# Kernel optimization log

Hardware: AMD Instinct MI355X
Metric: run time of the kernel (lower is better)

## Reference

```python
import jax, jax.numpy as jnp
import numpy as np

DIM = 256; HEADS = 8; DK = 64; DV = 64; FH = 32; FW = 32; B = 16
INK = HEADS * DK; INV = HEADS * DV; N = FH * FW
SCALE = DK ** -0.5; EPS = 1e-5


def _pos_indices():
    pos = np.stack(np.meshgrid(np.arange(FH), np.arange(FW), indexing='ij'), axis=-1).reshape(-1, 2)
    rel = np.abs(pos[:, None, :] - pos[None, :, :])  # [N,N,2]
    return jnp.asarray(rel[..., 0] * FW + rel[..., 1], jnp.int32)  # [N,N]


def _bn(x, g, b, m, v):
    # eval-mode BatchNorm2d over channel axis 1
    s = (g / jnp.sqrt(v + EPS))
    return x * s[None, :, None, None] + (b - m * s)[None, :, None, None]


def setup_inputs() -> dict:
    key = jax.random.key(0)
    ks = jax.random.split(key, 24)
    f32 = jnp.float32
    def bn_params(k, c):
        k1, k2, k3, k4 = jax.random.split(k, 4)
        return (jax.random.normal(k1, (c,), f32) * 0.1 + 1.0,
                jax.random.normal(k2, (c,), f32) * 0.1,
                jax.random.normal(k3, (c,), f32) * 0.1,
                jax.random.uniform(k4, (c,), f32) + 0.5)
    gq, bq, mq, vq = bn_params(ks[1], INK)
    gk, bk, mk, vk = bn_params(ks[3], INK)
    gv, bv, mv, vv = bn_params(ks[5], INV)
    go, bo, mo, vo = bn_params(ks[7], DIM)
    return {
        'x': jax.random.normal(ks[0], (B, DIM, FH, FW), f32),
        'wq': jax.random.normal(ks[2], (INK, DIM), f32) * (DIM ** -0.5),
        'gq': gq, 'bq': bq, 'mq': mq, 'vq': vq,
        'wk': jax.random.normal(ks[4], (INK, DIM), f32) * (DIM ** -0.5),
        'gk': gk, 'bk': bk, 'mk': mk, 'vk': vk,
        'wv': jax.random.normal(ks[6], (INV, DIM), f32) * (DIM ** -0.5),
        'gv': gv, 'bv': bv, 'mv': mv, 'vv': vv,
        'emb': jax.random.normal(ks[8], (N, HEADS), f32) * 0.02,
        'w_out': jax.random.normal(ks[9], (DIM, INV), f32) * (INV ** -0.5),
        'b_out': jax.random.normal(ks[10], (DIM,), f32) * 0.02,
        'go': go, 'bo': bo, 'mo': mo, 'vo': vo,
        'pos_indices': _pos_indices(),
    }


def reference(x, wq, gq, bq, mq, vq, wk, gk, bk, mk, vk, wv, gv, bv, mv, vv,
              emb, w_out, b_out, go, bo, mo, vo, pos_indices):
    b = x.shape[0]
    # 1x1 conv == channel matmul
    q = _bn(jnp.einsum('bchw,oc->bohw', x, wq), gq, bq, mq, vq)
    k = _bn(jnp.einsum('bchw,oc->bohw', x, wk), gk, bk, mk, vk)
    v = _bn(jnp.einsum('bchw,oc->bohw', x, wv), gv, bv, mv, vv)
    # 'b (h d) x y -> b h (x y) d'
    def split_heads(t, d):
        return t.reshape(b, HEADS, d, N).transpose(0, 1, 3, 2)
    q = split_heads(q, DK); k = split_heads(k, DK); v = split_heads(v, DV)
    dots = jnp.einsum('bhid,bhjd->bhij', q, k) * SCALE  # [b,h,N,N]
    bias = emb[pos_indices]                               # [N,N,h] gather
    dots = dots + jnp.transpose(bias, (2, 0, 1))[None] / SCALE
    attn = jax.nn.softmax(dots, axis=-1)
    out = jnp.einsum('bhij,bhjd->bhid', attn, v)
    out = out.transpose(0, 1, 3, 2).reshape(b, INV, FH, FW)  # 'b h (x y) d -> b (h d) x y'
    hs = out * jnp.clip(out + 3.0, 0.0, 6.0) / 6.0           # Hardswish
    y = jnp.einsum('bchw,oc->bohw', hs, w_out) + b_out[None, :, None, None]
    return _bn(y, go, bo, mo, vo)
```

## Files before the change

kernel.cpp:

```cpp
#include <hip/hip_runtime.h>

typedef __attribute__((ext_vector_type(4))) float f32x4;
typedef __attribute__((ext_vector_type(8))) _Float16 f16x8;
typedef __attribute__((ext_vector_type(4))) _Float16 f16x4;

static __device__ __forceinline__ f32x4 mfma16f(f16x8 a, f16x8 b, f32x4 c) {
    return __builtin_amdgcn_mfma_f32_16x16x32_f16(a, b, c, 0, 0, 0);
}

__global__ void split_w4(const float* __restrict__ s0, const float* __restrict__ s1,
                         const float* __restrict__ s2, const float* __restrict__ s3,
                         _Float16* __restrict__ d0h, _Float16* __restrict__ d0l,
                         _Float16* __restrict__ d1h, _Float16* __restrict__ d1l,
                         _Float16* __restrict__ d2h, _Float16* __restrict__ d2l,
                         _Float16* __restrict__ d3h, _Float16* __restrict__ d3l) {
    const int seg = blockIdx.x >> 9;
    const int i = (blockIdx.x & 511) * 256 + threadIdx.x;
    const float* src = (seg == 0) ? s0 : (seg == 1) ? s1 : (seg == 2) ? s2 : s3;
    _Float16* dh = (seg == 0) ? d0h : (seg == 1) ? d1h : (seg == 2) ? d2h : d3h;
    _Float16* dl = (seg == 0) ? d0l : (seg == 1) ? d1l : (seg == 2) ? d2l : d3l;
    const float f = src[i];
    const _Float16 h = (_Float16)f;
    dh[i] = h;
    dl[i] = (_Float16)(f - (float)h);
}

__global__ __launch_bounds__(256) void xsplit_t(
    const float* __restrict__ x, _Float16* __restrict__ xth, _Float16* __restrict__ xtl)
{
    __shared__ float lt[32][36];
    const int t = threadIdx.x;
    const int c0 = blockIdx.x * 32, hw0 = blockIdx.y * 32, b = blockIdx.z;
    {
        const int cl = t >> 3, hw4 = (t & 7) * 4;
        *(f32x4*)&lt[cl][hw4] = *(const f32x4*)&x[((size_t)(b * 256 + c0 + cl)) * 1024 + hw0 + hw4];
    }
    __syncthreads();
    {
        const int hwl = t >> 3, c4 = (t & 7) * 4;
        f16x4 hv, lv;
#pragma unroll
        for (int e = 0; e < 4; ++e) {
            const float f = lt[c4 + e][hwl];
            const _Float16 h = (_Float16)f;
            hv[e] = h;
            lv[e] = (_Float16)(f - (float)h);
        }
        const size_t off = ((size_t)(b * 1024 + hw0 + hwl)) * 256 + c0 + c4;
        *(f16x4*)(xth + off) = hv;
        *(f16x4*)(xtl + off) = lv;
    }
}

__global__ __launch_bounds__(256) void qkv_mfma(
    const _Float16* __restrict__ xth, const _Float16* __restrict__ xtl,
    const _Float16* __restrict__ wqh, const _Float16* __restrict__ wql,
    const _Float16* __restrict__ wkh, const _Float16* __restrict__ wkl,
    const _Float16* __restrict__ wvh, const _Float16* __restrict__ wvl,
    const float* __restrict__ gq, const float* __restrict__ bq, const float* __restrict__ mq, const float* __restrict__ vq,
    const float* __restrict__ gk, const float* __restrict__ bk, const float* __restrict__ mk, const float* __restrict__ vk,
    const float* __restrict__ gv, const float* __restrict__ bv, const float* __restrict__ mv, const float* __restrict__ vv,
    _Float16* __restrict__ qh, _Float16* __restrict__ ql,
    _Float16* __restrict__ kh, _Float16* __restrict__ kl,
    _Float16* __restrict__ vt)
{
    __shared__ _Float16 Ah[128][72];
    __shared__ _Float16 Al[128][72];
    __shared__ float sc_l[128], tc_l[128];

    const int t = threadIdx.x;
    const int bn = blockIdx.x;
    const int m0 = blockIdx.y * 128;
    const int proj = bn >> 2;
    const int o0 = (bn & 3) * 128;
    const int bimg = m0 >> 10;
    const int nb = m0 & 1023;

    const _Float16* Wh = (proj == 0) ? wqh : (proj == 1) ? wkh : wvh;
    const _Float16* Wl = (proj == 0) ? wql : (proj == 1) ? wkl : wvl;
    const float* G  = (proj == 0) ? gq : (proj == 1) ? gk : gv;
    const float* Bt = (proj == 0) ? bq : (proj == 1) ? bk : bv;
    const float* Mn = (proj == 0) ? mq : (proj == 1) ? mk : mv;
    const float* Vr = (proj == 0) ? vq : (proj == 1) ? vk : vv;

    if (t < 128) {
        const int o = o0 + t;
        float s = G[o] / sqrtf(Vr[o] + 1e-5f);
        float tt = Bt[o] - Mn[o] * s;
        if (proj == 0) { s *= 0.125f; tt *= 0.125f; }
        sc_l[t] = s; tc_l[t] = tt;
    }

    const int wave = t >> 6, lane = t & 63;
    const int quad = lane >> 4, l16 = lane & 15;
    const int wm = (wave >> 1) * 64, wn = (wave & 1) * 64;

    f32x4 acc[4][4] = {};

    for (int c0 = 0; c0 < 256; c0 += 64) {
        __syncthreads();
        {
            int r = t >> 3;
            const int cs = (t & 7) * 8;
#pragma unroll
            for (int p = 0; p < 4; ++p, r += 32) {
                const size_t off = ((size_t)(bimg * 1024 + nb + r)) * 256 + c0 + cs;
                *(f16x8*)&Ah[r][cs] = *(const f16x8*)(xth + off);
                *(f16x8*)&Al[r][cs] = *(const f16x8*)(xtl + off);
            }
        }
        __syncthreads();
#pragma unroll
        for (int kk = 0; kk < 2; ++kk) {
            f16x8 ah[4], al[4], bh[4], bl[4];
#pragma unroll
            for (int mi = 0; mi < 4; ++mi) {
                ah[mi] = *(const f16x8*)&Ah[wm + mi * 16 + l16][kk * 32 + quad * 8];
                al[mi] = *(const f16x8*)&Al[wm + mi * 16 + l16][kk * 32 + quad * 8];
            }
#pragma unroll
            for (int nj = 0; nj < 4; ++nj) {
                const size_t off = ((size_t)(o0 + wn + nj * 16 + l16)) * 256 + c0 + kk * 32 + quad * 8;
                bh[nj] = *(const f16x8*)(Wh + off);
                if (proj < 2) bl[nj] = *(const f16x8*)(Wl + off);
            }
            if (proj < 2) {
#pragma unroll
                for (int nj = 0; nj < 4; ++nj)
#pragma unroll
                    for (int mi = 0; mi < 4; ++mi) {
                        acc[nj][mi] = mfma16f(bh[nj], ah[mi], acc[nj][mi]);
                        acc[nj][mi] = mfma16f(bh[nj], al[mi], acc[nj][mi]);
                        acc[nj][mi] = mfma16f(bl[nj], ah[mi], acc[nj][mi]);
                    }
            } else {
#pragma unroll
                for (int mi = 0; mi < 4; ++mi)
#pragma unroll
                    for (int nj = 0; nj < 4; ++nj) {
                        acc[mi][nj] = mfma16f(ah[mi], bh[nj], acc[mi][nj]);
                        acc[mi][nj] = mfma16f(al[mi], bh[nj], acc[mi][nj]);
                    }
            }
        }
    }

    if (proj < 2) {
        _Float16* Oh = (proj == 0) ? qh : kh;
        _Float16* Ol = (proj == 0) ? ql : kl;
#pragma unroll
        for (int nj = 0; nj < 4; ++nj) {
            const int olb = wn + nj * 16 + quad * 4;
            const int ob = o0 + olb;
            const int head = ob >> 6, d0 = ob & 63;
#pragma unroll
            for (int mi = 0; mi < 4; ++mi) {
                const int n = nb + wm + mi * 16 + l16;
                f16x4 hv, lv;
#pragma unroll
                for (int rr = 0; rr < 4; ++rr) {
                    const float val = acc[nj][mi][rr] * sc_l[olb + rr] + tc_l[olb + rr];
                    const _Float16 h = (_Float16)val;
                    hv[rr] = h;
                    lv[rr] = (_Float16)(val - (float)h);
                }
                const size_t off = (((size_t)(bimg * 8 + head)) * 1024 + n) * 64 + d0;
                *(f16x4*)(Oh + off) = hv;
                *(f16x4*)(Ol + off) = lv;
            }
        }
    } else {
#pragma unroll
        for (int nj = 0; nj < 4; ++nj) {
            const int olb = wn + nj * 16 + l16;
            const int o = o0 + olb;
            const int head = o >> 6, d = o & 63;
            const float s = sc_l[olb], tt = tc_l[olb];
#pragma unroll
            for (int mi = 0; mi < 4; ++mi) {
                const int n0 = nb + wm + mi * 16 + quad * 4;
                f16x4 v4;
#pragma unroll
                for (int rr = 0; rr < 4; ++rr) v4[rr] = (_Float16)(acc[mi][nj][rr] * s + tt);
                *(f16x4*)(vt + (((size_t)(bimg * 8 + head)) * 64 + d) * 1024 + n0) = v4;
            }
        }
    }
}

__global__ __launch_bounds__(256, 3) void attn_mfma(
    const _Float16* __restrict__ qh, const _Float16* __restrict__ ql,
    const _Float16* __restrict__ kh, const _Float16* __restrict__ kl,
    const _Float16* __restrict__ vt,
    const float* __restrict__ emb,
    _Float16* __restrict__ hsh)
{
    __shared__ float    emb_s[1024];
    __shared__ _Float16 kth[64][72], ktl[64][72];
    __shared__ _Float16 vts[64][72];
    __shared__ _Float16 pt[128][76];

    const int t = threadIdx.x;
    const int bid = blockIdx.x;
    const int bh = bid & 127, qb = bid >> 7;
    const int b = bh >> 3, h = bh & 7;
    const int wave = t >> 6, lane = t & 63;
    const int quad = lane >> 4, l16 = lane & 15;
    const int q0 = qb * 128 + wave * 32;
    const float L2E = 1.44269504f;

    for (int i = t; i < 1024; i += 256) emb_s[i] = (8.0f * emb[i * 8 + h] - 12.0f) * L2E;

    const size_t base = (size_t)bh * 65536;

    f16x8 qfh[2][2], qfl[2][2];
#pragma unroll
    for (int mi = 0; mi < 2; ++mi)
#pragma unroll
        for (int kk = 0; kk < 2; ++kk) {
            const size_t off = base + (size_t)(q0 + mi * 16 + l16) * 64 + kk * 32 + quad * 8;
            qfh[mi][kk] = *(const f16x8*)(qh + off);
            qfl[mi][kk] = *(const f16x8*)(ql + off);
        }

    int xiv[2][4], dy0[2][4], dy1[2][4];
#pragma unroll
    for (int mi = 0; mi < 2; ++mi)
#pragma unroll
        for (int r = 0; r < 4; ++r) {
            const int ig = q0 + mi * 16 + quad * 4 + r;
            const int xi = ig >> 5, yi = ig & 31;
            xiv[mi][r] = xi;
            dy0[mi][r] = abs(yi - l16);
            dy1[mi][r] = abs(yi - 16 - l16);
        }

    const int sr = t >> 3;
    const int scs = (t & 7) * 8;
    const int rv = t >> 2;
    const int cv = (t & 3) * 16;

    f16x8 pkh[2], pkl[2], pvv[2];
#pragma unroll
    for (int p = 0; p < 2; ++p) {
        const size_t koff = base + (size_t)(p * 32 + sr) * 64 + scs;
        pkh[p] = *(const f16x8*)(kh + koff);
        pkl[p] = *(const f16x8*)(kl + koff);
        pvv[p] = *(const f16x8*)(vt + base + (size_t)rv * 1024 + cv + p * 8);
    }

    f32x4 ao[2][4] = {};
    float lsum[2][4] = {};

    for (int jb = 0; jb < 16; ++jb) {
        __syncthreads();
#pragma unroll
        for (int p = 0; p < 2; ++p) {
            *(f16x8*)&kth[p * 32 + sr][scs] = pkh[p];
            *(f16x8*)&ktl[p * 32 + sr][scs] = pkl[p];
            *(f16x8*)&vts[rv][cv + p * 8] = pvv[p];
        }
        __syncthreads();
        if (jb < 15) {
#pragma unroll
            for (int p = 0; p < 2; ++p) {
                const size_t koff = base + (size_t)((jb + 1) * 64 + p * 32 + sr) * 64 + scs;
                pkh[p] = *(const f16x8*)(kh + koff);
                pkl[p] = *(const f16x8*)(kl + koff);
                pvv[p] = *(const f16x8*)(vt + base + (size_t)rv * 1024 + (jb + 1) * 64 + cv + p * 8);
            }
        }

        f32x4 as[2][4] = {};
#pragma unroll
        for (int kk = 0; kk < 2; ++kk) {
            f16x8 kfh[4], kfl[4];
#pragma unroll
            for (int nj = 0; nj < 4; ++nj) {
                kfh[nj] = *(const f16x8*)&kth[nj * 16 + l16][kk * 32 + quad * 8];
                kfl[nj] = *(const f16x8*)&ktl[nj * 16 + l16][kk * 32 + quad * 8];
            }
#pragma unroll
            for (int mi = 0; mi < 2; ++mi)
#pragma unroll
                for (int nj = 0; nj < 4; ++nj) {
                    as[mi][nj] = mfma16f(qfh[mi][kk], kfh[nj], as[mi][nj]);
                    as[mi][nj] = mfma16f(qfh[mi][kk], kfl[nj], as[mi][nj]);
                    as[mi][nj] = mfma16f(qfl[mi][kk], kfh[nj], as[mi][nj]);
                }
        }

        const int xj0 = jb * 2, xj1 = jb * 2 + 1;
#pragma unroll
        for (int mi = 0; mi < 2; ++mi) {
#pragma unroll
            for (int r = 0; r < 4; ++r) {
                const int dxa = abs(xiv[mi][r] - xj0) << 5;
                const int dxb = abs(xiv[mi][r] - xj1) << 5;
                const int prow = wave * 32 + mi * 16 + quad * 4 + r;
                const float p0 = exp2f(fmaf(as[mi][0][r], L2E, emb_s[dxa + dy0[mi][r]]));
                const float p1 = exp2f(fmaf(as[mi][1][r], L2E, emb_s[dxa + dy1[mi][r]]));
                const float p2 = exp2f(fmaf(as[mi][2][r], L2E, emb_s[dxb + dy0[mi][r]]));
                const float p3 = exp2f(fmaf(as[mi][3][r], L2E, emb_s[dxb + dy1[mi][r]]));
                lsum[mi][r] += (p0 + p1) + (p2 + p3);
                pt[prow][0 * 16 + l16] = (_Float16)p0;
                pt[prow][1 * 16 + l16] = (_Float16)p1;
                pt[prow][2 * 16 + l16] = (_Float16)p2;
                pt[prow][3 * 16 + l16] = (_Float16)p3;
            }
        }

#pragma unroll
        for (int kk = 0; kk < 2; ++kk) {
            f16x8 pa[2], vf[4];
#pragma unroll
            for (int mi = 0; mi < 2; ++mi)
                pa[mi] = *(const f16x8*)&pt[wave * 32 + mi * 16 + l16][kk * 32 + quad * 8];
#pragma unroll
            for (int dj = 0; dj < 4; ++dj)
                vf[dj] = *(const f16x8*)&vts[dj * 16 + l16][kk * 32 + quad * 8];
#pragma unroll
            for (int mi = 0; mi < 2; ++mi)
#pragma unroll
                for (int dj = 0; dj < 4; ++dj)
                    ao[mi][dj] = mfma16f(pa[mi], vf[dj], ao[mi][dj]);
        }
    }

#pragma unroll
    for (int mi = 0; mi < 2; ++mi) {
#pragma unroll
        for (int r = 0; r < 4; ++r) {
            float l = lsum[mi][r];
#pragma unroll
            for (int msk = 1; msk < 16; msk <<= 1)
                l += __shfl_xor(l, msk, 64);
            const float inv = 1.0f / l;
            const int ig = q0 + mi * 16 + quad * 4 + r;
#pragma unroll
            for (int dj = 0; dj < 4; ++dj) {
                const float o = ao[mi][dj][r] * inv;
                const float hsw = o * fminf(fmaxf(o + 3.0f, 0.0f), 6.0f) * (1.0f / 6.0f);
                hsh[((size_t)(b * 1024 + ig)) * 512 + h * 64 + dj * 16 + l16] = (_Float16)hsw;
            }
        }
    }
}

__global__ __launch_bounds__(256) void out_mfma(
    const _Float16* __restrict__ hsh,
    const _Float16* __restrict__ woh, const _Float16* __restrict__ wol,
    const float* __restrict__ b_out, const float* __restrict__ go, const float* __restrict__ bo,
    const float* __restrict__ mo, const float* __restrict__ vo, float* __restrict__ y)
{
    __shared__ _Float16 Ah[64][136];

    const int t = threadIdx.x;
    const int m0 = blockIdx.x * 64;
    const int o0 = blockIdx.y * 128;
    const int bimg = m0 >> 10, nb = m0 & 1023;
    const int wave = t >> 6, lane = t & 63;
    const int quad = lane >> 4, l16 = lane & 15;
    const int wm = (wave >> 1) * 32, wn = (wave & 1) * 64;

    f32x4 acc[2][4] = {};

    for (int c0 = 0; c0 < 512; c0 += 128) {
        __syncthreads();
        {
            const int cs = (t & 7) * 16;
#pragma unroll
            for (int p = 0; p < 2; ++p) {
                const int r = (t >> 3) + p * 32;
                *(f16x8*)&Ah[r][cs]     = *(const f16x8*)(hsh + ((size_t)(m0 + r)) * 512 + c0 + cs);
                *(f16x8*)&Ah[r][cs + 8] = *(const f16x8*)(hsh + ((size_t)(m0 + r)) * 512 + c0 + cs + 8);
            }
        }
        __syncthreads();
#pragma unroll
        for (int kk = 0; kk < 4; ++kk) {
            f16x8 ah[2], bh[4], bl[4];
#pragma unroll
            for (int mi = 0; mi < 2; ++mi)
                ah[mi] = *(const f16x8*)&Ah[wm + mi * 16 + l16][kk * 32 + quad * 8];
#pragma unroll
            for (int nj = 0; nj < 4; ++nj) {
                const size_t off = ((size_t)(o0 + wn + nj * 16 + l16)) * 512 + c0 + kk * 32 + quad * 8;
                bh[nj] = *(const f16x8*)(woh + off);
                bl[nj] = *(const f16x8*)(wol + off);
            }
#pragma unroll
            for (int mi = 0; mi < 2; ++mi)
#pragma unroll
                for (int nj = 0; nj < 4; ++nj) {
                    acc[mi][nj] = mfma16f(ah[mi], bh[nj], acc[mi][nj]);
                    acc[mi][nj] = mfma16f(ah[mi], bl[nj], acc[mi][nj]);
                }
        }
    }

#pragma unroll
    for (int nj = 0; nj < 4; ++nj) {
        const int o = o0 + wn + nj * 16 + l16;
        const float s = go[o] / sqrtf(vo[o] + 1e-5f);
        const float tt = bo[o] - mo[o] * s;
        const float bf = b_out[o];
#pragma unroll
        for (int mi = 0; mi < 2; ++mi) {
            const int hw = nb + wm + mi * 16 + quad * 4;
            f32x4 v4;
#pragma unroll
            for (int rr = 0; rr < 4; ++rr) v4[rr] = (acc[mi][nj][rr] + bf) * s + tt;
            *(f32x4*)&y[((size_t)(bimg * 256 + o)) * 1024 + hw] = v4;
        }
    }
}

extern "C" void kernel_launch(void* const* d_in, const int* in_sizes, int n_in,
                              void* d_out, int out_size, void* d_ws, size_t ws_size,
                              hipStream_t stream) {
    const float* x     = (const float*)d_in[0];
    const float* wq    = (const float*)d_in[1];
    const float* gq    = (const float*)d_in[2];
    const float* bq    = (const float*)d_in[3];
    const float* mq    = (const float*)d_in[4];
    const float* vq    = (const float*)d_in[5];
    const float* wk    = (const float*)d_in[6];
    const float* gk    = (const float*)d_in[7];
    const float* bk    = (const float*)d_in[8];
    const float* mk    = (const float*)d_in[9];
    const float* vk    = (const float*)d_in[10];
    const float* wv    = (const float*)d_in[11];
    const float* gv    = (const float*)d_in[12];
    const float* bv    = (const float*)d_in[13];
    const float* mv    = (const float*)d_in[14];
    const float* vv    = (const float*)d_in[15];
    const float* emb   = (const float*)d_in[16];
    const float* w_out = (const float*)d_in[17];
    const float* b_out = (const float*)d_in[18];
    const float* go    = (const float*)d_in[19];
    const float* bo    = (const float*)d_in[20];
    const float* mo    = (const float*)d_in[21];
    const float* vo    = (const float*)d_in[22];

    _Float16* us = (_Float16*)d_ws;
    _Float16* xth = us;
    _Float16* xtl = us + 4194304;
    _Float16* hsh = us;
    _Float16* wsp = us + 16777216;
    _Float16* wqh = wsp,            *wql = wsp + 131072;
    _Float16* wkh = wsp + 262144,   *wkl = wsp + 393216;
    _Float16* wvh = wsp + 524288,   *wvl = wsp + 655360;
    _Float16* woh = wsp + 786432,   *wol = wsp + 917504;
    _Float16* qv  = us + 17825792;
    _Float16* qhw = qv,             *qlw = qv + 8388608;
    _Float16* khw = qv + 16777216,  *klw = qv + 25165824;
    _Float16* vtw = qv + 33554432;

    split_w4<<<2048, 256, 0, stream>>>(wq, wk, wv, w_out,
                                       wqh, wql, wkh, wkl, wvh, wvl, woh, wol);

    xsplit_t<<<dim3(8, 32, 16), 256, 0, stream>>>(x, xth, xtl);

    qkv_mfma<<<dim3(12, 128), 256, 0, stream>>>(
        xth, xtl, wqh, wql, wkh, wkl, wvh, wvl,
        gq, bq, mq, vq, gk, bk, mk, vk, gv, bv, mv, vv,
        qhw, qlw, khw, klw, vtw);

    attn_mfma<<<1024, 256, 0, stream>>>(
        qhw, qlw, khw, klw, vtw, emb, hsh);

    out_mfma<<<dim3(256, 2), 256, 0, stream>>>(
        hsh, woh, wol, b_out, go, bo, mo, vo, (float*)d_out);
}
```

Baseline: 332.9 us.

## Drop K low-part split in attention, merge prep kernels, prefetch out weights

```diff
diff --git a/kernel.cpp b/kernel.cpp
--- a/kernel.cpp
+++ b/kernel.cpp
@@ -8,47 +8,51 @@
     return __builtin_amdgcn_mfma_f32_16x16x32_f16(a, b, c, 0, 0, 0);
 }
 
-__global__ void split_w4(const float* __restrict__ s0, const float* __restrict__ s1,
-                         const float* __restrict__ s2, const float* __restrict__ s3,
-                         _Float16* __restrict__ d0h, _Float16* __restrict__ d0l,
-                         _Float16* __restrict__ d1h, _Float16* __restrict__ d1l,
-                         _Float16* __restrict__ d2h, _Float16* __restrict__ d2l,
-                         _Float16* __restrict__ d3h, _Float16* __restrict__ d3l) {
-    const int seg = blockIdx.x >> 9;
-    const int i = (blockIdx.x & 511) * 256 + threadIdx.x;
-    const float* src = (seg == 0) ? s0 : (seg == 1) ? s1 : (seg == 2) ? s2 : s3;
-    _Float16* dh = (seg == 0) ? d0h : (seg == 1) ? d1h : (seg == 2) ? d2h : d3h;
-    _Float16* dl = (seg == 0) ? d0l : (seg == 1) ? d1l : (seg == 2) ? d2l : d3l;
-    const float f = src[i];
-    const _Float16 h = (_Float16)f;
-    dh[i] = h;
-    dl[i] = (_Float16)(f - (float)h);
-}
-
-__global__ __launch_bounds__(256) void xsplit_t(
-    const float* __restrict__ x, _Float16* __restrict__ xth, _Float16* __restrict__ xtl)
+__global__ __launch_bounds__(256) void prep(
+    const float* __restrict__ x,
+    const float* __restrict__ s0, const float* __restrict__ s1,
+    const float* __restrict__ s2, const float* __restrict__ s3,
+    _Float16* __restrict__ d0h, _Float16* __restrict__ d0l,
+    _Float16* __restrict__ d1h, _Float16* __restrict__ d1l,
+    _Float16* __restrict__ d2h, _Float16* __restrict__ d2l,
+    _Float16* __restrict__ d3h, _Float16* __restrict__ d3l,
+    _Float16* __restrict__ xth, _Float16* __restrict__ xtl)
 {
     __shared__ float lt[32][36];
     const int t = threadIdx.x;
-    const int c0 = blockIdx.x * 32, hw0 = blockIdx.y * 32, b = blockIdx.z;
-    {
-        const int cl = t >> 3, hw4 = (t & 7) * 4;
-        *(f32x4*)&lt[cl][hw4] = *(const f32x4*)&x[((size_t)(b * 256 + c0 + cl)) * 1024 + hw0 + hw4];
-    }
-    __syncthreads();
-    {
-        const int hwl = t >> 3, c4 = (t & 7) * 4;
-        f16x4 hv, lv;
-#pragma unroll
-        for (int e = 0; e < 4; ++e) {
-            const float f = lt[c4 + e][hwl];
-            const _Float16 h = (_Float16)f;
-            hv[e] = h;
-            lv[e] = (_Float16)(f - (float)h);
-        }
-        const size_t off = ((size_t)(b * 1024 + hw0 + hwl)) * 256 + c0 + c4;
-        *(f16x4*)(xth + off) = hv;
-        *(f16x4*)(xtl + off) = lv;
+    const int bid = blockIdx.x;
+    if (bid < 2048) {
+        const int seg = bid >> 9;
+        const int i = (bid & 511) * 256 + t;
+        const float* src = (seg == 0) ? s0 : (seg == 1) ? s1 : (seg == 2) ? s2 : s3;
+        _Float16* dh = (seg == 0) ? d0h : (seg == 1) ? d1h : (seg == 2) ? d2h : d3h;
+        _Float16* dl = (seg == 0) ? d0l : (seg == 1) ? d1l : (seg == 2) ? d2l : d3l;
+        const float f = src[i];
+        const _Float16 h = (_Float16)f;
+        dh[i] = h;
+        dl[i] = (_Float16)(f - (float)h);
+    } else {
+        const int bid2 = bid - 2048;
+        const int c0 = (bid2 & 7) * 32, hw0 = ((bid2 >> 3) & 31) * 32, b = bid2 >> 8;
+        {
+            const int cl = t >> 3, hw4 = (t & 7) * 4;
+            *(f32x4*)&lt[cl][hw4] = *(const f32x4*)&x[((size_t)(b * 256 + c0 + cl)) * 1024 + hw0 + hw4];
+        }
+        __syncthreads();
+        {
+            const int hwl = t >> 3, c4 = (t & 7) * 4;
+            f16x4 hv, lv;
+#pragma unroll
+            for (int e = 0; e < 4; ++e) {
+                const float f = lt[c4 + e][hwl];
+                const _Float16 h = (_Float16)f;
+                hv[e] = h;
+                lv[e] = (_Float16)(f - (float)h);
+            }
+            const size_t off = ((size_t)(b * 1024 + hw0 + hwl)) * 256 + c0 + c4;
+            *(f16x4*)(xth + off) = hv;
+            *(f16x4*)(xtl + off) = lv;
+        }
     }
 }
 
@@ -61,7 +65,7 @@
     const float* __restrict__ gk, const float* __restrict__ bk, const float* __restrict__ mk, const float* __restrict__ vk,
     const float* __restrict__ gv, const float* __restrict__ bv, const float* __restrict__ mv, const float* __restrict__ vv,
     _Float16* __restrict__ qh, _Float16* __restrict__ ql,
-    _Float16* __restrict__ kh, _Float16* __restrict__ kl,
+    _Float16* __restrict__ kh,
     _Float16* __restrict__ vt)
 {
     __shared__ _Float16 Ah[128][72];
@@ -147,7 +151,6 @@
 
     if (proj < 2) {
         _Float16* Oh = (proj == 0) ? qh : kh;
-        _Float16* Ol = (proj == 0) ? ql : kl;
 #pragma unroll
         for (int nj = 0; nj < 4; ++nj) {
             const int olb = wn + nj * 16 + quad * 4;
@@ -166,7 +169,7 @@
                 }
                 const size_t off = (((size_t)(bimg * 8 + head)) * 1024 + n) * 64 + d0;
                 *(f16x4*)(Oh + off) = hv;
-                *(f16x4*)(Ol + off) = lv;
+                if (proj == 0) *(f16x4*)(ql + off) = lv;
             }
         }
     } else {
@@ -190,14 +193,14 @@
 
 __global__ __launch_bounds__(256, 3) void attn_mfma(
     const _Float16* __restrict__ qh, const _Float16* __restrict__ ql,
-    const _Float16* __restrict__ kh, const _Float16* __restrict__ kl,
+    const _Float16* __restrict__ kh,
     const _Float16* __restrict__ vt,
     const float* __restrict__ emb,
     _Float16* __restrict__ hsh)
 {
     __shared__ float    emb_s[1024];
-    __shared__ _Float16 kth[64][72], ktl[64][72];
-    __shared__ _Float16 vts[64][72];
+    __shared__ _Float16 kth[64][76];
+    __shared__ _Float16 vts[64][76];
     __shared__ _Float16 pt[128][76];
 
     const int t = threadIdx.x;
@@ -240,12 +243,10 @@
     const int rv = t >> 2;
     const int cv = (t & 3) * 16;
 
-    f16x8 pkh[2], pkl[2], pvv[2];
+    f16x8 pkh[2], pvv[2];
 #pragma unroll
     for (int p = 0; p < 2; ++p) {
-        const size_t koff = base + (size_t)(p * 32 + sr) * 64 + scs;
-        pkh[p] = *(const f16x8*)(kh + koff);
-        pkl[p] = *(const f16x8*)(kl + koff);
+        pkh[p] = *(const f16x8*)(kh + base + (size_t)(p * 32 + sr) * 64 + scs);
         pvv[p] = *(const f16x8*)(vt + base + (size_t)rv * 1024 + cv + p * 8);
     }
 
@@ -257,16 +258,13 @@
 #pragma unroll
         for (int p = 0; p < 2; ++p) {
             *(f16x8*)&kth[p * 32 + sr][scs] = pkh[p];
-            *(f16x8*)&ktl[p * 32 + sr][scs] = pkl[p];
             *(f16x8*)&vts[rv][cv + p * 8] = pvv[p];
         }
         __syncthreads();
         if (jb < 15) {
 #pragma unroll
             for (int p = 0; p < 2; ++p) {
-                const size_t koff = base + (size_t)((jb + 1) * 64 + p * 32 + sr) * 64 + scs;
-                pkh[p] = *(const f16x8*)(kh + koff);
-                pkl[p] = *(const f16x8*)(kl + koff);
+                pkh[p] = *(const f16x8*)(kh + base + (size_t)((jb + 1) * 64 + p * 32 + sr) * 64 + scs);
                 pvv[p] = *(const f16x8*)(vt + base + (size_t)rv * 1024 + (jb + 1) * 64 + cv + p * 8);
             }
         }
@@ -274,18 +272,15 @@
         f32x4 as[2][4] = {};
 #pragma unroll
         for (int kk = 0; kk < 2; ++kk) {
-            f16x8 kfh[4], kfl[4];
-#pragma unroll
-            for (int nj = 0; nj < 4; ++nj) {
+            f16x8 kfh[4];
+#pragma unroll
+            for (int nj = 0; nj < 4; ++nj)
                 kfh[nj] = *(const f16x8*)&kth[nj * 16 + l16][kk * 32 + quad * 8];
-                kfl[nj] = *(const f16x8*)&ktl[nj * 16 + l16][kk * 32 + quad * 8];
-            }
 #pragma unroll
             for (int mi = 0; mi < 2; ++mi)
 #pragma unroll
                 for (int nj = 0; nj < 4; ++nj) {
                     as[mi][nj] = mfma16f(qfh[mi][kk], kfh[nj], as[mi][nj]);
-                    as[mi][nj] = mfma16f(qfh[mi][kk], kfl[nj], as[mi][nj]);
                     as[mi][nj] = mfma16f(qfl[mi][kk], kfh[nj], as[mi][nj]);
                 }
         }
@@ -364,10 +359,20 @@
     const int wm = (wave >> 1) * 32, wn = (wave & 1) * 64;
 
     f32x4 acc[2][4] = {};
-
-    for (int c0 = 0; c0 < 512; c0 += 128) {
-        __syncthreads();
-        {
+    f16x8 bh[4], bl[4], nbh[4], nbl[4];
+
+#pragma unroll
+    for (int nj = 0; nj < 4; ++nj) {
+        const size_t off = ((size_t)(o0 + wn + nj * 16 + l16)) * 512 + quad * 8;
+        bh[nj] = *(const f16x8*)(woh + off);
+        bl[nj] = *(const f16x8*)(wol + off);
+    }
+
+#pragma unroll
+    for (int it = 0; it < 16; ++it) {
+        const int c0 = (it >> 2) * 128, kk = it & 3;
+        if (kk == 0) {
+            __syncthreads();
             const int cs = (t & 7) * 16;
 #pragma unroll
             for (int p = 0; p < 2; ++p) {
@@ -375,28 +380,31 @@
                 *(f16x8*)&Ah[r][cs]     = *(const f16x8*)(hsh + ((size_t)(m0 + r)) * 512 + c0 + cs);
                 *(f16x8*)&Ah[r][cs + 8] = *(const f16x8*)(hsh + ((size_t)(m0 + r)) * 512 + c0 + cs + 8);
             }
-        }
-        __syncthreads();
-#pragma unroll
-        for (int kk = 0; kk < 4; ++kk) {
-            f16x8 ah[2], bh[4], bl[4];
-#pragma unroll
-            for (int mi = 0; mi < 2; ++mi)
-                ah[mi] = *(const f16x8*)&Ah[wm + mi * 16 + l16][kk * 32 + quad * 8];
+            __syncthreads();
+        }
+        if (it < 15) {
+            const int nit = it + 1;
+            const int nc0 = (nit >> 2) * 128, nkk = nit & 3;
 #pragma unroll
             for (int nj = 0; nj < 4; ++nj) {
-                const size_t off = ((size_t)(o0 + wn + nj * 16 + l16)) * 512 + c0 + kk * 32 + quad * 8;
-                bh[nj] = *(const f16x8*)(woh + off);
-                bl[nj] = *(const f16x8*)(wol + off);
-            }
-#pragma unroll
-            for (int mi = 0; mi < 2; ++mi)
-#pragma unroll
-                for (int nj = 0; nj < 4; ++nj) {
-                    acc[mi][nj] = mfma16f(ah[mi], bh[nj], acc[mi][nj]);
-                    acc[mi][nj] = mfma16f(ah[mi], bl[nj], acc[mi][nj]);
-                }
-        }
+                const size_t off = ((size_t)(o0 + wn + nj * 16 + l16)) * 512 + nc0 + nkk * 32 + quad * 8;
+                nbh[nj] = *(const f16x8*)(woh + off);
+                nbl[nj] = *(const f16x8*)(wol + off);
+            }
+        }
+        f16x8 ah[2];
+#pragma unroll
+        for (int mi = 0; mi < 2; ++mi)
+            ah[mi] = *(const f16x8*)&Ah[wm + mi * 16 + l16][kk * 32 + quad * 8];
+#pragma unroll
+        for (int mi = 0; mi < 2; ++mi)
+#pragma unroll
+            for (int nj = 0; nj < 4; ++nj) {
+                acc[mi][nj] = mfma16f(ah[mi], bh[nj], acc[mi][nj]);
+                acc[mi][nj] = mfma16f(ah[mi], bl[nj], acc[mi][nj]);
+            }
+#pragma unroll
+        for (int nj = 0; nj < 4; ++nj) { bh[nj] = nbh[nj]; bl[nj] = nbl[nj]; }
     }
 
 #pragma unroll
@@ -454,21 +462,20 @@
     _Float16* woh = wsp + 786432,   *wol = wsp + 917504;
     _Float16* qv  = us + 17825792;
     _Float16* qhw = qv,             *qlw = qv + 8388608;
-    _Float16* khw = qv + 16777216,  *klw = qv + 25165824;
+    _Float16* khw = qv + 16777216;
     _Float16* vtw = qv + 33554432;
 
-    split_w4<<<2048, 256, 0, stream>>>(wq, wk, wv, w_out,
-                                       wqh, wql, wkh, wkl, wvh, wvl, woh, wol);
-
-    xsplit_t<<<dim3(8, 32, 16), 256, 0, stream>>>(x, xth, xtl);
+    prep<<<6144, 256, 0, stream>>>(x, wq, wk, wv, w_out,
+                                   wqh, wql, wkh, wkl, wvh, wvl, woh, wol,
+                                   xth, xtl);
 
     qkv_mfma<<<dim3(12, 128), 256, 0, stream>>>(
         xth, xtl, wqh, wql, wkh, wkl, wvh, wvl,
         gq, bq, mq, vq, gk, bk, mk, vk, gv, bv, mv, vv,
-        qhw, qlw, khw, klw, vtw);
+        qhw, qlw, khw, vtw);
 
     attn_mfma<<<1024, 256, 0, stream>>>(
-        qhw, qlw, khw, klw, vtw, emb, hsh);
+        qhw, qlw, khw, vtw, emb, hsh);
 
     out_mfma<<<dim3(256, 2), 256, 0, stream>>>(
         hsh, woh, wol, b_out, go, bo, mo, vo, (float*)d_out);
```

Result: faster. 302.8 us (-9.1%).
